# Optimization experiments

Measured on AMD Instinct MI355X. Metric: run time of the kernel, lower is better.

## Reference

```python
import jax, jax.numpy as jnp
import numpy as np

EMB_DIM = 128
MID = 192  # ceil(1.5 * emb_dim)
VOCAB = 3000
KCLS = 5
B = 16
S = 128
EPS = 1e-5


def _linear_init(k, fin, fout):
    k1, k2 = jax.random.split(k)
    bound = 1.0 / np.sqrt(fin)
    W = jax.random.uniform(k1, (fin, fout), minval=-bound, maxval=bound, dtype=jnp.float32)
    b = jax.random.uniform(k2, (fout,), minval=-bound, maxval=bound, dtype=jnp.float32)
    return W, b


def setup_inputs() -> dict:
    key = jax.random.key(0)
    ks = jax.random.split(key, 7)
    emb = jax.random.normal(ks[0], (VOCAB, EMB_DIM), dtype=jnp.float32)
    W1, b1 = _linear_init(ks[1], 2 * EMB_DIM, MID)   # encoder layer 1
    W2, b2 = _linear_init(ks[2], MID, EMB_DIM)       # encoder layer 2
    W3, b3 = _linear_init(ks[3], EMB_DIM, MID)       # decoder layer 1
    W4, b4 = _linear_init(ks[4], MID, 2 * EMB_DIM)   # decoder layer 2
    Wk, bk = _linear_init(ks[5], EMB_DIM, KCLS)      # soft head
    inputs = jax.random.randint(ks[6], (B, S), 0, VOCAB, dtype=jnp.int64)
    return dict(inputs=inputs, emb=emb, W1=W1, b1=b1, W2=W2, b2=b2,
                W3=W3, b3=b3, W4=W4, b4=b4, Wk=Wk, bk=bk)


def _forward(inputs, emb, W1, b1, W2, b2, W3, b3, W4, b4, Wk, bk):
    X = emb[inputs]                      # (B,S,m)
    Bs, Sl, m = X.shape
    bidx = jnp.arange(Bs)
    karr = jnp.arange(Sl)
    jarr = jnp.arange(Sl - 1)

    def step(carry, t):
        nodes, counts, acc = carry       # (B,S,m), (B,S), (B,)
        L = Sl - t                       # current active list length
        right, left = nodes[:, 1:], nodes[:, :-1]          # pair j = (node[j+1], node[j])
        y = (jnp.concatenate([right, left], -1) @ W1 + b1) @ W2 + b2   # (B,S-1,m)
        xx = (y @ W3 + b3) @ W4 + b4                                    # (B,S-1,2m)
        # torch cross_entropy with float-vector target: -sum(target * log_softmax(input))
        ls1 = -(right * jax.nn.log_softmax(xx[..., :m], -1)).sum(-1)
        ls2 = -(left * jax.nn.log_softmax(xx[..., m:], -1)).sum(-1)
        n1, n2 = counts[:, 1:], counts[:, :-1]
        loss = ((n1 + EPS) * ls1 + (n2 + EPS) * ls2) / (n1 + n2 + EPS)
        valid = jarr < (L - 1)                                          # only first L-1 pairs active
        idx = jnp.argmin(jnp.where(valid[None, :], loss, jnp.inf), axis=1)  # (B,)
        acc = acc + jnp.take_along_axis(loss, idx[:, None], 1)[:, 0]
        father_x = jnp.take_along_axis(y, idx[:, None, None], 1)[:, 0]  # (B,m)
        # faithful bug: lc = nodelist[idx-1] (python wrap to L-1 when idx==0), rc = nodelist[idx]
        lc_idx = jnp.where(idx == 0, L - 1, idx - 1)
        father_cnt = (jnp.take_along_axis(counts, idx[:, None], 1)[:, 0]
                      + jnp.take_along_axis(counts, lc_idx[:, None], 1)[:, 0])
        pos = jnp.maximum(idx - 1, 0)
        # new list: drop lc and rc, father lands at pos; gather map reproduces list insert/remove
        src = jnp.where((idx[:, None] == 0) | (karr[None, :] < idx[:, None] - 1),
                        karr[None, :], karr[None, :] + 1)
        src = jnp.minimum(src, Sl - 1)
        nodes = jnp.take_along_axis(nodes, src[:, :, None], 1).at[bidx, pos].set(father_x)
        counts = jnp.take_along_axis(counts, src, 1).at[bidx, pos].set(father_cnt)
        return (nodes, counts, acc), None

    init = (X, jnp.ones((Bs, Sl), X.dtype), jnp.zeros((Bs,), X.dtype))
    (nodes, counts, acc), _ = jax.lax.scan(step, init, jnp.arange(Sl - 1))
    pred = jnp.argmax(nodes[:, 0] @ Wk + bk, axis=-1)   # argmax softmax == argmax logits
    return pred, acc.sum() / Bs


def reference(inputs, emb, W1, b1, W2, b2, W3, b3, W4, b4, Wk, bk):
    return _forward(inputs, emb, W1, b1, W2, b2, W3, b3, W4, b4, Wk, bk)
```

## Files before the change

### kernel.cpp

```cpp
#include <hip/hip_runtime.h>
#include <math.h>

#define EMB 128
#define MID 192
#define SEQ 128
#define BATCH 16
#define NPAIR 127
#define KCLS 5
#define EPSF 1e-5f

#define OFF_WYT   0
#define OFF_BY    32768
#define OFF_WXX   32896
#define OFF_BXX   65664
#define OFF_NODES 65920
#define OFF_YC    328064
#define OFF_L0    588160

__global__ void k_comp(const float* __restrict__ W1, const float* __restrict__ b1,
                       const float* __restrict__ W2, const float* __restrict__ b2,
                       const float* __restrict__ W3, const float* __restrict__ b3,
                       const float* __restrict__ W4, const float* __restrict__ b4,
                       float* __restrict__ ws) {
    int tid = blockIdx.x * blockDim.x + threadIdx.x;
    if (tid < 32768) {
        int k = tid >> 7, o = tid & 127;
        float a = 0.f;
        for (int j = 0; j < MID; ++j) a += W1[k*MID+j] * W2[j*EMB+o];
        int q8 = k >> 5, jj = k & 31;
        ws[OFF_WYT + ((q8*128 + o) << 5) + jj] = a;
    } else if (tid < 65536) {
        int t = tid - 32768;
        int k = t >> 8, c = t & 255;
        float a = 0.f;
        for (int j = 0; j < MID; ++j) a += W3[k*MID+j] * W4[j*256+c];
        int h4 = k >> 5, jj = k & 31;
        ws[OFF_WXX + ((h4*256 + c) << 5) + jj] = a;
    } else if (tid < 65536 + 128) {
        int o = tid - 65536;
        float a = b2[o];
        for (int j = 0; j < MID; ++j) a += b1[j] * W2[j*EMB+o];
        ws[OFF_BY + o] = a;
    } else if (tid < 65536 + 128 + 256) {
        int o = tid - 65536 - 128;
        float a = b4[o];
        for (int j = 0; j < MID; ++j) a += b3[j] * W4[j*256+o];
        ws[OFF_BXX + o] = a;
    }
}

__global__ void k_nodes(const int* __restrict__ inp, const float* __restrict__ emb,
                        float* __restrict__ ws) {
    int tid = blockIdx.x * blockDim.x + threadIdx.x;
    if (tid >= BATCH*SEQ*EMB) return;
    int d = tid & 127;
    int bs = tid >> 7;
    int tok = inp[bs];
    ws[OFF_NODES + tid] = emb[tok*EMB + d];
}

__global__ void __launch_bounds__(1024) k_init(float* __restrict__ ws) {
    __shared__ float s_x[2][2*EMB];
    __shared__ float s_red[8][2][EMB];
    __shared__ float s_redx[4][2][256];
    __shared__ float s_y[2][EMB];
    __shared__ float s_by[EMB];
    __shared__ float s_bxx[2*EMB];
    __shared__ float s_ls[2][2];
    int tid = threadIdx.x;
    int b = blockIdx.x >> 4, g = blockIdx.x & 15;
    float4 wy8[8], wxx8[8];
    {
        const float4* gw = (const float4*)(ws + OFF_WYT) + (size_t)tid*8;
        #pragma unroll
        for (int i = 0; i < 8; ++i) wy8[i] = gw[i];
        const float4* gx = (const float4*)(ws + OFF_WXX) + (size_t)tid*8;
        #pragma unroll
        for (int i = 0; i < 8; ++i) wxx8[i] = gx[i];
    }
    if (tid < EMB) s_by[tid] = ws[OFF_BY + tid];
    if (tid < 2*EMB) s_bxx[tid] = ws[OFF_BXX + tid];
    const float* nodes = ws + OFF_NODES + (size_t)b*SEQ*EMB;
    float* yc = ws + OFF_YC + (size_t)b*NPAIR*EMB;
    int q8 = tid >> 7, o = tid & 127;
    int h4 = tid >> 8, c = tid & 255;
    __syncthreads();
    for (int it = 0; it < 4; ++it) {
        int base = g*8 + it*2;
        if (tid < 512) {
            int p_s = tid >> 8, kk = tid & 255;
            int j = base + p_s;
            int jj = j < NPAIR ? j : NPAIR - 1;
            s_x[p_s][kk] = nodes[(jj + (kk < 128 ? 1 : 0))*EMB + (kk & 127)];
        }
        __syncthreads();
        {
            const float4* sx4 = (const float4*)s_x;
            float a0 = 0.f, a1 = 0.f;
            #pragma unroll
            for (int i = 0; i < 8; ++i) {
                float4 w = wy8[i];
                float4 x0 = sx4[q8*8 + i];
                float4 x1 = sx4[64 + q8*8 + i];
                a0 += x0.x*w.x + x0.y*w.y + x0.z*w.z + x0.w*w.w;
                a1 += x1.x*w.x + x1.y*w.y + x1.z*w.z + x1.w*w.w;
            }
            s_red[q8][0][o] = a0;
            s_red[q8][1][o] = a1;
        }
        __syncthreads();
        if (tid < 256) {
            int p = tid >> 7, oo = tid & 127;
            float yv = s_by[oo];
            #pragma unroll
            for (int q = 0; q < 8; ++q) yv += s_red[q][p][oo];
            s_y[p][oo] = yv;
            int j2 = base + p;
            if (j2 < NPAIR) yc[(size_t)j2*EMB + oo] = yv;
        }
        __syncthreads();
        {
            const float4* sy4 = (const float4*)s_y;
            float c0 = 0.f, c1 = 0.f;
            #pragma unroll
            for (int i = 0; i < 8; ++i) {
                float4 w = wxx8[i];
                float4 y0 = sy4[h4*8 + i];
                float4 y1 = sy4[32 + h4*8 + i];
                c0 += y0.x*w.x + y0.y*w.y + y0.z*w.z + y0.w*w.w;
                c1 += y1.x*w.x + y1.y*w.y + y1.z*w.z + y1.w*w.w;
            }
            s_redx[h4][0][c] = c0;
            s_redx[h4][1][c] = c1;
        }
        __syncthreads();
        if (tid < 256) {
            int w = tid >> 6, lane = tid & 63;
            int p2 = w >> 1, h2 = w & 1;
            int cA = h2*128 + lane, cB = cA + 64;
            float v0 = s_redx[0][p2][cA] + s_redx[1][p2][cA] + s_redx[2][p2][cA] + s_redx[3][p2][cA] + s_bxx[cA];
            float v1 = s_redx[0][p2][cB] + s_redx[1][p2][cB] + s_redx[2][p2][cB] + s_redx[3][p2][cB] + s_bxx[cB];
            float m = fmaxf(v0, v1);
            for (int s = 32; s; s >>= 1) m = fmaxf(m, __shfl_xor(m, s, 64));
            float se = expf(v0 - m) + expf(v1 - m);
            for (int s = 32; s; s >>= 1) se += __shfl_xor(se, s, 64);
            float lse = m + logf(se);
            float o0 = s_x[p2][cA], o1 = s_x[p2][cB];
            float term = o0*(v0 - lse) + o1*(v1 - lse);
            for (int s = 32; s; s >>= 1) term += __shfl_xor(term, s, 64);
            if (lane == 0) s_ls[p2][h2] = -term;
        }
        __syncthreads();
        if (tid < 2) {
            int j2 = base + tid;
            if (j2 < NPAIR) {
                float l = ((1.f+EPSF)*s_ls[tid][0] + (1.f+EPSF)*s_ls[tid][1]) / (2.f + EPSF);
                ws[OFF_L0 + b*NPAIR + j2] = l;
            }
        }
        __syncthreads();
    }
}

__global__ void __launch_bounds__(1024) k_seq(float* __restrict__ ws,
                      const float* __restrict__ Wk, const float* __restrict__ bkv,
                      float* __restrict__ out) {
    __shared__ float s_nodes[SEQ*EMB];
    __shared__ float s_yc[NPAIR*EMB];
    __shared__ float s_red[8][2][EMB];
    __shared__ float s_redx[4][2][256];
    __shared__ float s_y[2][EMB];
    __shared__ float s_by[EMB];
    __shared__ float s_bxx[2*EMB];
    __shared__ float s_ls[2][2];
    __shared__ float s_loss[2][NPAIR];
    __shared__ float s_cnt[2][SEQ];
    __shared__ int   s_nslot[2][SEQ];
    __shared__ int   s_yslot[2][NPAIR];
    __shared__ int   s_q[2];
    __shared__ float s_wv[2];
    __shared__ int   s_wi[2];
    __shared__ float s_log[KCLS];

    int tid = threadIdx.x;
    int b = blockIdx.x;
    float4 wy8[8], wxx8[8];
    {
        const float4* gw = (const float4*)(ws + OFF_WYT) + (size_t)tid*8;
        #pragma unroll
        for (int i = 0; i < 8; ++i) wy8[i] = gw[i];
        const float4* gx = (const float4*)(ws + OFF_WXX) + (size_t)tid*8;
        #pragma unroll
        for (int i = 0; i < 8; ++i) wxx8[i] = gx[i];
    }
    {
        const float4* gn = (const float4*)(ws + OFF_NODES + (size_t)b*SEQ*EMB);
        float4* sn = (float4*)s_nodes;
        for (int i = tid; i < SEQ*EMB/4; i += 1024) sn[i] = gn[i];
        const float4* gy = (const float4*)(ws + OFF_YC + (size_t)b*NPAIR*EMB);
        float4* sy = (float4*)s_yc;
        for (int i = tid; i < NPAIR*EMB/4; i += 1024) sy[i] = gy[i];
    }
    if (tid < EMB) s_by[tid] = ws[OFF_BY + tid];
    if (tid < 2*EMB) s_bxx[tid] = ws[OFF_BXX + tid];
    if (tid < NPAIR) { s_loss[0][tid] = ws[OFF_L0 + b*NPAIR + tid]; s_yslot[0][tid] = tid; }
    if (tid < SEQ)   { s_cnt[0][tid] = 1.f; s_nslot[0][tid] = tid; }
    float acc = 0.f;
    int q8 = tid >> 7, o = tid & 127;
    int h4 = tid >> 8, c = tid & 255;
    __syncthreads();

    #pragma unroll 1
    for (int t = 0; t < NPAIR; ++t) {
        int L = SEQ - t;
        int cur = t & 1, nxt = cur ^ 1;
        if (t > 0) {
            {
                int r = (q8 < 4) ? 1 : 0;
                int slot0 = s_nslot[cur][s_q[0] + r];
                int slot1 = s_nslot[cur][s_q[1] + r];
                const float4* n4 = (const float4*)s_nodes;
                int sub = (q8 & 3) * 8;
                int base0 = slot0*32 + sub;
                int base1 = slot1*32 + sub;
                float a0 = 0.f, a1 = 0.f;
                #pragma unroll
                for (int i = 0; i < 8; ++i) {
                    float4 w = wy8[i];
                    float4 x0 = n4[base0 + i];
                    float4 x1 = n4[base1 + i];
                    a0 += x0.x*w.x + x0.y*w.y + x0.z*w.z + x0.w*w.w;
                    a1 += x1.x*w.x + x1.y*w.y + x1.z*w.z + x1.w*w.w;
                }
                s_red[q8][0][o] = a0;
                s_red[q8][1][o] = a1;
            }
            __syncthreads();
            if (tid < 256) {
                int p = tid >> 7, oo = tid & 127;
                float yv = s_by[oo];
                #pragma unroll
                for (int q = 0; q < 8; ++q) yv += s_red[q][p][oo];
                s_y[p][oo] = yv;
                s_yc[(size_t)s_yslot[cur][s_q[p]]*EMB + oo] = yv;
            }
            __syncthreads();
            {
                const float4* sy4 = (const float4*)s_y;
                float c0 = 0.f, c1 = 0.f;
                #pragma unroll
                for (int i = 0; i < 8; ++i) {
                    float4 w = wxx8[i];
                    float4 y0 = sy4[h4*8 + i];
                    float4 y1 = sy4[32 + h4*8 + i];
                    c0 += y0.x*w.x + y0.y*w.y + y0.z*w.z + y0.w*w.w;
                    c1 += y1.x*w.x + y1.y*w.y + y1.z*w.z + y1.w*w.w;
                }
                s_redx[h4][0][c] = c0;
                s_redx[h4][1][c] = c1;
            }
            __syncthreads();
            if (tid < 256) {
                int w = tid >> 6, lane = tid & 63;
                int p2 = w >> 1, h2 = w & 1;
                int cA = h2*128 + lane, cB = cA + 64;
                float v0 = s_redx[0][p2][cA] + s_redx[1][p2][cA] + s_redx[2][p2][cA] + s_redx[3][p2][cA] + s_bxx[cA];
                float v1 = s_redx[0][p2][cB] + s_redx[1][p2][cB] + s_redx[2][p2][cB] + s_redx[3][p2][cB] + s_bxx[cB];
                float m = fmaxf(v0, v1);
                for (int s = 32; s; s >>= 1) m = fmaxf(m, __shfl_xor(m, s, 64));
                float se = expf(v0 - m) + expf(v1 - m);
                for (int s = 32; s; s >>= 1) se += __shfl_xor(se, s, 64);
                float lse = m + logf(se);
                int slot = s_nslot[cur][s_q[p2] + (h2 == 0 ? 1 : 0)];
                float o0 = s_nodes[slot*EMB + lane];
                float o1 = s_nodes[slot*EMB + 64 + lane];
                float term = o0*(v0 - lse) + o1*(v1 - lse);
                for (int s = 32; s; s >>= 1) term += __shfl_xor(term, s, 64);
                if (lane == 0) s_ls[p2][h2] = -term;
            }
            __syncthreads();
        }
        if (tid < 128) {
            float v = INFINITY;
            if (tid < L-1) {
                v = s_loss[cur][tid];
                if (t > 0 && (tid == s_q[0] || tid == s_q[1])) {
                    int which = (tid == s_q[0]) ? 0 : 1;
                    float n1 = s_cnt[cur][tid+1], n2 = s_cnt[cur][tid];
                    v = ((n1+EPSF)*s_ls[which][0] + (n2+EPSF)*s_ls[which][1]) / (n1+n2+EPSF);
                    s_loss[cur][tid] = v;
                }
            }
            int ii = tid;
            for (int s = 32; s; s >>= 1) {
                float ov = __shfl_xor(v, s, 64);
                int   oi = __shfl_xor(ii, s, 64);
                if (ov < v || (ov == v && oi < ii)) { v = ov; ii = oi; }
            }
            if ((tid & 63) == 0) { s_wv[tid>>6] = v; s_wi[tid>>6] = ii; }
        }
        __syncthreads();
        {
            float bv0 = s_wv[0], bv1 = s_wv[1];
            int idx = (bv1 < bv0) ? s_wi[1] : s_wi[0];
            if (tid == 0) acc += fminf(bv0, bv1);
            int pos = idx > 0 ? idx - 1 : 0;
            bool doShift = (idx > 0);
            if (tid < 128) {
                int sC = (doShift && tid >= pos+1 && tid <= L-2) ? 1 : 0;
                float nc = s_cnt[cur][tid + sC];
                int   nn = s_nslot[cur][tid + sC];
                if (tid == pos) {
                    float fcnt = s_cnt[cur][idx] + s_cnt[cur][idx == 0 ? L-1 : idx-1];
                    nc = fcnt;
                }
                s_cnt[nxt][tid] = nc;
                s_nslot[nxt][tid] = nn;
                if (tid < NPAIR) {
                    int sL = (doShift && tid >= pos+1 && tid <= L-3) ? 1 : 0;
                    s_loss[nxt][tid]  = s_loss[cur][tid + sL];
                    s_yslot[nxt][tid] = s_yslot[cur][tid + sL];
                }
            } else if (tid < 256) {
                int d = tid - 128;
                int slotF = s_nslot[cur][pos];
                int ysI   = s_yslot[cur][idx];
                s_nodes[slotF*EMB + d] = s_yc[(size_t)ysI*EMB + d];
            } else if (tid == 256) {
                s_q[0] = (pos >= 1) ? pos - 1 : pos;
                s_q[1] = pos;
            }
        }
        __syncthreads();
    }
    if (tid < KCLS) {
        int slot0 = s_nslot[1][0];
        float a = bkv[tid];
        for (int k = 0; k < EMB; ++k) a += s_nodes[slot0*EMB + k] * Wk[k*KCLS + tid];
        s_log[tid] = a;
    }
    __syncthreads();
    if (tid == 0) {
        int best = 0;
        for (int cc = 1; cc < KCLS; ++cc) if (s_log[cc] > s_log[best]) best = cc;
        out[b] = (float)best;
        atomicAdd(&out[BATCH], acc * (1.f/16.f));
    }
}

extern "C" void kernel_launch(void* const* d_in, const int* in_sizes, int n_in,
                              void* d_out, int out_size, void* d_ws, size_t ws_size,
                              hipStream_t stream) {
    const int*   inp = (const int*)d_in[0];
    const float* emb = (const float*)d_in[1];
    const float* W1  = (const float*)d_in[2];
    const float* b1  = (const float*)d_in[3];
    const float* W2  = (const float*)d_in[4];
    const float* b2  = (const float*)d_in[5];
    const float* W3  = (const float*)d_in[6];
    const float* b3  = (const float*)d_in[7];
    const float* W4  = (const float*)d_in[8];
    const float* b4  = (const float*)d_in[9];
    const float* Wk  = (const float*)d_in[10];
    const float* bk  = (const float*)d_in[11];
    float* out = (float*)d_out;
    float* ws  = (float*)d_ws;

    hipMemsetAsync(d_out, 0, (size_t)out_size * sizeof(float), stream);

    k_comp<<<(65920 + 255) / 256, 256, 0, stream>>>(W1, b1, W2, b2, W3, b3, W4, b4, ws);
    k_nodes<<<(BATCH*SEQ*EMB + 255) / 256, 256, 0, stream>>>(inp, emb, ws);
    k_init<<<BATCH * 16, 1024, 0, stream>>>(ws);
    k_seq<<<BATCH, 1024, 0, stream>>>(ws, Wk, bk, out);
}
```

Baseline: 560.4 us.

## Decompose pair linear maps into per-node projections cached per slot

The composed encoder and decoder weights are split by input half, so each node gets cached left/right encoder projections and left/right decoder logit projections. A pair's y and logits then become sums of two per-node vectors plus a bias. In the sequential loop only the new father node is projected, using a single fused 128x768 matvec, instead of re-running two pair matvecs with cross-warp reductions. This removes one matvec stage and several barriers per step, but adds global-memory reads of cached projections in the critical loop, extra precompute kernels, and changes the floating-point summation order.

```diff
diff --git a/kernel.cpp b/kernel.cpp
--- a/kernel.cpp
+++ b/kernel.cpp
@@ -9,271 +9,243 @@
 #define KCLS 5
 #define EPSF 1e-5f
 
-#define OFF_WYT   0
-#define OFF_BY    32768
-#define OFF_WXX   32896
-#define OFF_BXX   65664
-#define OFF_NODES 65920
-#define OFF_YC    328064
-#define OFF_L0    588160
-
-__global__ void k_comp(const float* __restrict__ W1, const float* __restrict__ b1,
-                       const float* __restrict__ W2, const float* __restrict__ b2,
-                       const float* __restrict__ W3, const float* __restrict__ b3,
-                       const float* __restrict__ W4, const float* __restrict__ b4,
-                       float* __restrict__ ws) {
+#define OFF_WBIG  0
+#define OFF_BY    98304
+#define OFF_BXX2  98432
+#define OFF_WY    98688
+#define OFF_WXX   131456
+#define OFF_BXX   164224
+#define OFF_NODES 164480
+#define OFF_L0    426624
+#define OFF_L     428656
+#define OFF_R     690800
+#define OFF_UL    952944
+#define OFF_UR    1477232
+
+__global__ void k_comp1(const float* __restrict__ W1, const float* __restrict__ b1,
+                        const float* __restrict__ W2, const float* __restrict__ b2,
+                        const float* __restrict__ W3, const float* __restrict__ b3,
+                        const float* __restrict__ W4, const float* __restrict__ b4,
+                        const int* __restrict__ inp, const float* __restrict__ emb,
+                        float* __restrict__ ws) {
     int tid = blockIdx.x * blockDim.x + threadIdx.x;
     if (tid < 32768) {
         int k = tid >> 7, o = tid & 127;
         float a = 0.f;
         for (int j = 0; j < MID; ++j) a += W1[k*MID+j] * W2[j*EMB+o];
-        int q8 = k >> 5, jj = k & 31;
-        ws[OFF_WYT + ((q8*128 + o) << 5) + jj] = a;
+        ws[OFF_WY + k*128 + o] = a;
+        if (k >= 128) ws[OFF_WBIG + o*128 + (k-128)] = a;
+        else          ws[OFF_WBIG + (128+o)*128 + k] = a;
     } else if (tid < 65536) {
         int t = tid - 32768;
         int k = t >> 8, c = t & 255;
         float a = 0.f;
         for (int j = 0; j < MID; ++j) a += W3[k*MID+j] * W4[j*256+c];
-        int h4 = k >> 5, jj = k & 31;
-        ws[OFF_WXX + ((h4*256 + c) << 5) + jj] = a;
-    } else if (tid < 65536 + 128) {
+        ws[OFF_WXX + k*256 + c] = a;
+    } else if (tid < 65664) {
         int o = tid - 65536;
         float a = b2[o];
         for (int j = 0; j < MID; ++j) a += b1[j] * W2[j*EMB+o];
         ws[OFF_BY + o] = a;
-    } else if (tid < 65536 + 128 + 256) {
-        int o = tid - 65536 - 128;
+    } else if (tid < 65920) {
+        int o = tid - 65664;
         float a = b4[o];
         for (int j = 0; j < MID; ++j) a += b3[j] * W4[j*256+o];
         ws[OFF_BXX + o] = a;
-    }
-}
-
-__global__ void k_nodes(const int* __restrict__ inp, const float* __restrict__ emb,
-                        float* __restrict__ ws) {
+    } else if (tid < 65920 + BATCH*SEQ*EMB) {
+        int t2 = tid - 65920;
+        int d = t2 & 127, bs = t2 >> 7;
+        int tok = inp[bs];
+        ws[OFF_NODES + t2] = emb[tok*EMB + d];
+    }
+}
+
+__global__ void k_comp2(float* __restrict__ ws) {
     int tid = blockIdx.x * blockDim.x + threadIdx.x;
-    if (tid >= BATCH*SEQ*EMB) return;
-    int d = tid & 127;
-    int bs = tid >> 7;
-    int tok = inp[bs];
-    ws[OFF_NODES + tid] = emb[tok*EMB + d];
-}
-
-__global__ void __launch_bounds__(1024) k_init(float* __restrict__ ws) {
-    __shared__ float s_x[2][2*EMB];
-    __shared__ float s_red[8][2][EMB];
-    __shared__ float s_redx[4][2][256];
-    __shared__ float s_y[2][EMB];
-    __shared__ float s_by[EMB];
-    __shared__ float s_bxx[2*EMB];
-    __shared__ float s_ls[2][2];
+    if (tid < 32768) {
+        int k = tid >> 8, c = tid & 255;
+        float a = 0.f;
+        for (int m = 0; m < 128; ++m) a += ws[OFF_WY + (128+k)*128 + m] * ws[OFF_WXX + m*256 + c];
+        ws[OFF_WBIG + (256+c)*128 + k] = a;
+    } else if (tid < 65536) {
+        int t = tid - 32768;
+        int k = t >> 8, c = t & 255;
+        float a = 0.f;
+        for (int m = 0; m < 128; ++m) a += ws[OFF_WY + k*128 + m] * ws[OFF_WXX + m*256 + c];
+        ws[OFF_WBIG + (512+c)*128 + k] = a;
+    } else if (tid < 65792) {
+        int c = tid - 65536;
+        float a = ws[OFF_BXX + c];
+        for (int m = 0; m < 128; ++m) a += ws[OFF_BY + m] * ws[OFF_WXX + m*256 + c];
+        ws[OFF_BXX2 + c] = a;
+    }
+}
+
+__global__ void __launch_bounds__(768) k_cache(float* __restrict__ ws) {
+    __shared__ float s_x[EMB];
     int tid = threadIdx.x;
     int b = blockIdx.x >> 4, g = blockIdx.x & 15;
-    float4 wy8[8], wxx8[8];
+    float4 wb[32];
     {
-        const float4* gw = (const float4*)(ws + OFF_WYT) + (size_t)tid*8;
+        const float4* gw = (const float4*)(ws + OFF_WBIG) + (size_t)tid*32;
         #pragma unroll
-        for (int i = 0; i < 8; ++i) wy8[i] = gw[i];
-        const float4* gx = (const float4*)(ws + OFF_WXX) + (size_t)tid*8;
+        for (int i = 0; i < 32; ++i) wb[i] = gw[i];
+    }
+    const float* gnod = ws + OFF_NODES + (size_t)b*SEQ*EMB;
+    float* gL  = ws + OFF_L  + (size_t)b*SEQ*EMB;
+    float* gR  = ws + OFF_R  + (size_t)b*SEQ*EMB;
+    float* gUL = ws + OFF_UL + (size_t)b*SEQ*256;
+    float* gUR = ws + OFF_UR + (size_t)b*SEQ*256;
+    for (int i = 0; i < 8; ++i) {
+        int n = g*8 + i;
+        if (tid < EMB) s_x[tid] = gnod[n*EMB + tid];
+        __syncthreads();
+        float a0=0.f,a1=0.f,a2=0.f,a3=0.f;
+        const float4* f4 = (const float4*)s_x;
         #pragma unroll
-        for (int i = 0; i < 8; ++i) wxx8[i] = gx[i];
-    }
-    if (tid < EMB) s_by[tid] = ws[OFF_BY + tid];
-    if (tid < 2*EMB) s_bxx[tid] = ws[OFF_BXX + tid];
-    const float* nodes = ws + OFF_NODES + (size_t)b*SEQ*EMB;
-    float* yc = ws + OFF_YC + (size_t)b*NPAIR*EMB;
-    int q8 = tid >> 7, o = tid & 127;
-    int h4 = tid >> 8, c = tid & 255;
+        for (int ii = 0; ii < 8; ++ii) {
+            float4 w0 = wb[4*ii+0], x0 = f4[4*ii+0];
+            float4 w1 = wb[4*ii+1], x1 = f4[4*ii+1];
+            float4 w2 = wb[4*ii+2], x2 = f4[4*ii+2];
+            float4 w3 = wb[4*ii+3], x3 = f4[4*ii+3];
+            a0 += w0.x*x0.x + w0.y*x0.y + w0.z*x0.z + w0.w*x0.w;
+            a1 += w1.x*x1.x + w1.y*x1.y + w1.z*x1.z + w1.w*x1.w;
+            a2 += w2.x*x2.x + w2.y*x2.y + w2.z*x2.z + w2.w*x2.w;
+            a3 += w3.x*x3.x + w3.y*x3.y + w3.z*x3.z + w3.w*x3.w;
+        }
+        float o = (a0+a1)+(a2+a3);
+        if      (tid < 128) gL [n*EMB + tid]        = o;
+        else if (tid < 256) gR [n*EMB + tid-128]    = o;
+        else if (tid < 512) gUL[n*256 + tid-256]    = o;
+        else                gUR[n*256 + tid-512]    = o;
+        __syncthreads();
+    }
+}
+
+__global__ void __launch_bounds__(128) k_loss(float* __restrict__ ws) {
+    __shared__ float s_ls[2];
+    int tid = threadIdx.x;
+    int b = blockIdx.x / NPAIR, j = blockIdx.x % NPAIR;
+    int h2 = tid >> 6, lane = tid & 63;
+    const float* gUL = ws + OFF_UL + (size_t)b*SEQ*256;
+    const float* gUR = ws + OFF_UR + (size_t)b*SEQ*256;
+    const float* gnod = ws + OFF_NODES + (size_t)b*SEQ*EMB;
+    int cA = h2*128 + lane, cB = cA + 64;
+    float v0 = gUL[j*256+cA] + gUR[(j+1)*256+cA] + ws[OFF_BXX2+cA];
+    float v1 = gUL[j*256+cB] + gUR[(j+1)*256+cB] + ws[OFF_BXX2+cB];
+    float m = fmaxf(v0, v1);
+    for (int s = 32; s; s >>= 1) m = fmaxf(m, __shfl_xor(m, s, 64));
+    float se = expf(v0 - m) + expf(v1 - m);
+    for (int s = 32; s; s >>= 1) se += __shfl_xor(se, s, 64);
+    float lse = m + logf(se);
+    int slotD = j + (h2 == 0 ? 1 : 0);
+    float o0 = gnod[slotD*EMB + lane];
+    float o1 = gnod[slotD*EMB + 64 + lane];
+    float term = o0*(v0 - lse) + o1*(v1 - lse);
+    for (int s = 32; s; s >>= 1) term += __shfl_xor(term, s, 64);
+    if (lane == 0) s_ls[h2] = -term;
     __syncthreads();
-    for (int it = 0; it < 4; ++it) {
-        int base = g*8 + it*2;
-        if (tid < 512) {
-            int p_s = tid >> 8, kk = tid & 255;
-            int j = base + p_s;
-            int jj = j < NPAIR ? j : NPAIR - 1;
-            s_x[p_s][kk] = nodes[(jj + (kk < 128 ? 1 : 0))*EMB + (kk & 127)];
-        }
-        __syncthreads();
-        {
-            const float4* sx4 = (const float4*)s_x;
-            float a0 = 0.f, a1 = 0.f;
-            #pragma unroll
-            for (int i = 0; i < 8; ++i) {
-                float4 w = wy8[i];
-                float4 x0 = sx4[q8*8 + i];
-                float4 x1 = sx4[64 + q8*8 + i];
-                a0 += x0.x*w.x + x0.y*w.y + x0.z*w.z + x0.w*w.w;
-                a1 += x1.x*w.x + x1.y*w.y + x1.z*w.z + x1.w*w.w;
-            }
-            s_red[q8][0][o] = a0;
-            s_red[q8][1][o] = a1;
-        }
-        __syncthreads();
-        if (tid < 256) {
-            int p = tid >> 7, oo = tid & 127;
-            float yv = s_by[oo];
-            #pragma unroll
-            for (int q = 0; q < 8; ++q) yv += s_red[q][p][oo];
-            s_y[p][oo] = yv;
-            int j2 = base + p;
-            if (j2 < NPAIR) yc[(size_t)j2*EMB + oo] = yv;
-        }
-        __syncthreads();
-        {
-            const float4* sy4 = (const float4*)s_y;
-            float c0 = 0.f, c1 = 0.f;
-            #pragma unroll
-            for (int i = 0; i < 8; ++i) {
-                float4 w = wxx8[i];
-                float4 y0 = sy4[h4*8 + i];
-                float4 y1 = sy4[32 + h4*8 + i];
-                c0 += y0.x*w.x + y0.y*w.y + y0.z*w.z + y0.w*w.w;
-                c1 += y1.x*w.x + y1.y*w.y + y1.z*w.z + y1.w*w.w;
-            }
-            s_redx[h4][0][c] = c0;
-            s_redx[h4][1][c] = c1;
-        }
-        __syncthreads();
-        if (tid < 256) {
-            int w = tid >> 6, lane = tid & 63;
-            int p2 = w >> 1, h2 = w & 1;
-            int cA = h2*128 + lane, cB = cA + 64;
-            float v0 = s_redx[0][p2][cA] + s_redx[1][p2][cA] + s_redx[2][p2][cA] + s_redx[3][p2][cA] + s_bxx[cA];
-            float v1 = s_redx[0][p2][cB] + s_redx[1][p2][cB] + s_redx[2][p2][cB] + s_redx[3][p2][cB] + s_bxx[cB];
-            float m = fmaxf(v0, v1);
-            for (int s = 32; s; s >>= 1) m = fmaxf(m, __shfl_xor(m, s, 64));
-            float se = expf(v0 - m) + expf(v1 - m);
-            for (int s = 32; s; s >>= 1) se += __shfl_xor(se, s, 64);
-            float lse = m + logf(se);
-            float o0 = s_x[p2][cA], o1 = s_x[p2][cB];
-            float term = o0*(v0 - lse) + o1*(v1 - lse);
-            for (int s = 32; s; s >>= 1) term += __shfl_xor(term, s, 64);
-            if (lane == 0) s_ls[p2][h2] = -term;
-        }
-        __syncthreads();
-        if (tid < 2) {
-            int j2 = base + tid;
-            if (j2 < NPAIR) {
-                float l = ((1.f+EPSF)*s_ls[tid][0] + (1.f+EPSF)*s_ls[tid][1]) / (2.f + EPSF);
-                ws[OFF_L0 + b*NPAIR + j2] = l;
-            }
-        }
-        __syncthreads();
-    }
-}
-
-__global__ void __launch_bounds__(1024) k_seq(float* __restrict__ ws,
+    if (tid == 0) {
+        float l = ((1.f+EPSF)*s_ls[0] + (1.f+EPSF)*s_ls[1]) / (2.f + EPSF);
+        ws[OFF_L0 + b*NPAIR + j] = l;
+    }
+}
+
+__global__ void __launch_bounds__(768) k_seq(float* __restrict__ ws,
                       const float* __restrict__ Wk, const float* __restrict__ bkv,
                       float* __restrict__ out) {
     __shared__ float s_nodes[SEQ*EMB];
-    __shared__ float s_yc[NPAIR*EMB];
-    __shared__ float s_red[8][2][EMB];
-    __shared__ float s_redx[4][2][256];
-    __shared__ float s_y[2][EMB];
+    __shared__ float s_father[EMB];
+    __shared__ float s_Lf[EMB];
+    __shared__ float s_Rf[EMB];
+    __shared__ float s_ULf[256];
+    __shared__ float s_URf[256];
     __shared__ float s_by[EMB];
-    __shared__ float s_bxx[2*EMB];
+    __shared__ float s_bxx2[256];
     __shared__ float s_ls[2][2];
     __shared__ float s_loss[2][NPAIR];
     __shared__ float s_cnt[2][SEQ];
     __shared__ int   s_nslot[2][SEQ];
-    __shared__ int   s_yslot[2][NPAIR];
     __shared__ int   s_q[2];
+    __shared__ int   s_sFb[2];
     __shared__ float s_wv[2];
     __shared__ int   s_wi[2];
     __shared__ float s_log[KCLS];
 
     int tid = threadIdx.x;
     int b = blockIdx.x;
-    float4 wy8[8], wxx8[8];
+    float4 wb[32];
     {
-        const float4* gw = (const float4*)(ws + OFF_WYT) + (size_t)tid*8;
+        const float4* gw = (const float4*)(ws + OFF_WBIG) + (size_t)tid*32;
         #pragma unroll
-        for (int i = 0; i < 8; ++i) wy8[i] = gw[i];
-        const float4* gx = (const float4*)(ws + OFF_WXX) + (size_t)tid*8;
-        #pragma unroll
-        for (int i = 0; i < 8; ++i) wxx8[i] = gx[i];
-    }
+        for (int i = 0; i < 32; ++i) wb[i] = gw[i];
+    }
+    float* gnod = ws + OFF_NODES + (size_t)b*SEQ*EMB;
+    float* gL  = ws + OFF_L  + (size_t)b*SEQ*EMB;
+    float* gR  = ws + OFF_R  + (size_t)b*SEQ*EMB;
+    float* gUL = ws + OFF_UL + (size_t)b*SEQ*256;
+    float* gUR = ws + OFF_UR + (size_t)b*SEQ*256;
     {
-        const float4* gn = (const float4*)(ws + OFF_NODES + (size_t)b*SEQ*EMB);
+        const float4* gn4 = (const float4*)gnod;
         float4* sn = (float4*)s_nodes;
-        for (int i = tid; i < SEQ*EMB/4; i += 1024) sn[i] = gn[i];
-        const float4* gy = (const float4*)(ws + OFF_YC + (size_t)b*NPAIR*EMB);
-        float4* sy = (float4*)s_yc;
-        for (int i = tid; i < NPAIR*EMB/4; i += 1024) sy[i] = gy[i];
+        for (int i = tid; i < SEQ*EMB/4; i += 768) sn[i] = gn4[i];
     }
     if (tid < EMB) s_by[tid] = ws[OFF_BY + tid];
-    if (tid < 2*EMB) s_bxx[tid] = ws[OFF_BXX + tid];
-    if (tid < NPAIR) { s_loss[0][tid] = ws[OFF_L0 + b*NPAIR + tid]; s_yslot[0][tid] = tid; }
-    if (tid < SEQ)   { s_cnt[0][tid] = 1.f; s_nslot[0][tid] = tid; }
+    if (tid < 256) s_bxx2[tid] = ws[OFF_BXX2 + tid];
+    if (tid < NPAIR) s_loss[0][tid] = ws[OFF_L0 + b*NPAIR + tid];
+    if (tid < SEQ) { s_cnt[0][tid] = 1.f; s_nslot[0][tid] = tid; }
+    if (tid == 0) { s_sFb[0] = -1; s_sFb[1] = -1; }
     float acc = 0.f;
-    int q8 = tid >> 7, o = tid & 127;
-    int h4 = tid >> 8, c = tid & 255;
     __syncthreads();
 
     #pragma unroll 1
     for (int t = 0; t < NPAIR; ++t) {
         int L = SEQ - t;
-        int cur = t & 1, nxt = cur ^ 1;
+        int cur = t & 1;
+        int prevPar = (t + 1) & 1;
+        int sF = s_sFb[prevPar];
         if (t > 0) {
             {
-                int r = (q8 < 4) ? 1 : 0;
-                int slot0 = s_nslot[cur][s_q[0] + r];
-                int slot1 = s_nslot[cur][s_q[1] + r];
-                const float4* n4 = (const float4*)s_nodes;
-                int sub = (q8 & 3) * 8;
-                int base0 = slot0*32 + sub;
-                int base1 = slot1*32 + sub;
-                float a0 = 0.f, a1 = 0.f;
+                float a0=0.f,a1=0.f,a2=0.f,a3=0.f;
+                const float4* f4 = (const float4*)s_father;
                 #pragma unroll
-                for (int i = 0; i < 8; ++i) {
-                    float4 w = wy8[i];
-                    float4 x0 = n4[base0 + i];
-                    float4 x1 = n4[base1 + i];
-                    a0 += x0.x*w.x + x0.y*w.y + x0.z*w.z + x0.w*w.w;
-                    a1 += x1.x*w.x + x1.y*w.y + x1.z*w.z + x1.w*w.w;
+                for (int ii = 0; ii < 8; ++ii) {
+                    float4 w0 = wb[4*ii+0], x0 = f4[4*ii+0];
+                    float4 w1 = wb[4*ii+1], x1 = f4[4*ii+1];
+                    float4 w2 = wb[4*ii+2], x2 = f4[4*ii+2];
+                    float4 w3 = wb[4*ii+3], x3 = f4[4*ii+3];
+                    a0 += w0.x*x0.x + w0.y*x0.y + w0.z*x0.z + w0.w*x0.w;
+                    a1 += w1.x*x1.x + w1.y*x1.y + w1.z*x1.z + w1.w*x1.w;
+                    a2 += w2.x*x2.x + w2.y*x2.y + w2.z*x2.z + w2.w*x2.w;
+                    a3 += w3.x*x3.x + w3.y*x3.y + w3.z*x3.z + w3.w*x3.w;
                 }
-                s_red[q8][0][o] = a0;
-                s_red[q8][1][o] = a1;
-            }
-            __syncthreads();
-            if (tid < 256) {
-                int p = tid >> 7, oo = tid & 127;
-                float yv = s_by[oo];
-                #pragma unroll
-                for (int q = 0; q < 8; ++q) yv += s_red[q][p][oo];
-                s_y[p][oo] = yv;
-                s_yc[(size_t)s_yslot[cur][s_q[p]]*EMB + oo] = yv;
-            }
-            __syncthreads();
-            {
-                const float4* sy4 = (const float4*)s_y;
-                float c0 = 0.f, c1 = 0.f;
-                #pragma unroll
-                for (int i = 0; i < 8; ++i) {
-                    float4 w = wxx8[i];
-                    float4 y0 = sy4[h4*8 + i];
-                    float4 y1 = sy4[32 + h4*8 + i];
-                    c0 += y0.x*w.x + y0.y*w.y + y0.z*w.z + y0.w*w.w;
-                    c1 += y1.x*w.x + y1.y*w.y + y1.z*w.z + y1.w*w.w;
-                }
-                s_redx[h4][0][c] = c0;
-                s_redx[h4][1][c] = c1;
+                float o = (a0+a1)+(a2+a3);
+                if      (tid < 128) { gL [sF*EMB + tid]      = o; s_Lf [tid]     = o; }
+                else if (tid < 256) { gR [sF*EMB + tid-128]  = o; s_Rf [tid-128] = o; }
+                else if (tid < 512) { gUL[sF*256 + tid-256]  = o; s_ULf[tid-256] = o; }
+                else                { gUR[sF*256 + tid-512]  = o; s_URf[tid-512] = o; }
             }
             __syncthreads();
             if (tid < 256) {
                 int w = tid >> 6, lane = tid & 63;
                 int p2 = w >> 1, h2 = w & 1;
+                int q = s_q[p2];
+                int slotL = s_nslot[cur][q], slotR = s_nslot[cur][q+1];
                 int cA = h2*128 + lane, cB = cA + 64;
-                float v0 = s_redx[0][p2][cA] + s_redx[1][p2][cA] + s_redx[2][p2][cA] + s_redx[3][p2][cA] + s_bxx[cA];
-                float v1 = s_redx[0][p2][cB] + s_redx[1][p2][cB] + s_redx[2][p2][cB] + s_redx[3][p2][cB] + s_bxx[cB];
+                float ulA = (slotL == sF) ? s_ULf[cA] : gUL[slotL*256 + cA];
+                float ulB = (slotL == sF) ? s_ULf[cB] : gUL[slotL*256 + cB];
+                float urA = (slotR == sF) ? s_URf[cA] : gUR[slotR*256 + cA];
+                float urB = (slotR == sF) ? s_URf[cB] : gUR[slotR*256 + cB];
+                float v0 = ulA + urA + s_bxx2[cA];
+                float v1 = ulB + urB + s_bxx2[cB];
                 float m = fmaxf(v0, v1);
                 for (int s = 32; s; s >>= 1) m = fmaxf(m, __shfl_xor(m, s, 64));
                 float se = expf(v0 - m) + expf(v1 - m);
                 for (int s = 32; s; s >>= 1) se += __shfl_xor(se, s, 64);
                 float lse = m + logf(se);
-                int slot = s_nslot[cur][s_q[p2] + (h2 == 0 ? 1 : 0)];
-                float o0 = s_nodes[slot*EMB + lane];
-                float o1 = s_nodes[slot*EMB + 64 + lane];
+                int slotD = (h2 == 0) ? slotR : slotL;
+                float o0 = s_nodes[slotD*EMB + lane];
+                float o1 = s_nodes[slotD*EMB + 64 + lane];
                 float term = o0*(v0 - lse) + o1*(v1 - lse);
                 for (int s = 32; s; s >>= 1) term += __shfl_xor(term, s, 64);
                 if (lane == 0) s_ls[p2][h2] = -term;
@@ -305,30 +277,33 @@
             int idx = (bv1 < bv0) ? s_wi[1] : s_wi[0];
             if (tid == 0) acc += fminf(bv0, bv1);
             int pos = idx > 0 ? idx - 1 : 0;
+            int nxt = cur ^ 1;
             bool doShift = (idx > 0);
             if (tid < 128) {
                 int sC = (doShift && tid >= pos+1 && tid <= L-2) ? 1 : 0;
                 float nc = s_cnt[cur][tid + sC];
                 int   nn = s_nslot[cur][tid + sC];
-                if (tid == pos) {
-                    float fcnt = s_cnt[cur][idx] + s_cnt[cur][idx == 0 ? L-1 : idx-1];
-                    nc = fcnt;
-                }
+                if (tid == pos) nc = s_cnt[cur][idx] + s_cnt[cur][idx == 0 ? L-1 : idx-1];
                 s_cnt[nxt][tid] = nc;
                 s_nslot[nxt][tid] = nn;
                 if (tid < NPAIR) {
                     int sL = (doShift && tid >= pos+1 && tid <= L-3) ? 1 : 0;
-                    s_loss[nxt][tid]  = s_loss[cur][tid + sL];
-                    s_yslot[nxt][tid] = s_yslot[cur][tid + sL];
+                    s_loss[nxt][tid] = s_loss[cur][tid + sL];
                 }
             } else if (tid < 256) {
                 int d = tid - 128;
-                int slotF = s_nslot[cur][pos];
-                int ysI   = s_yslot[cur][idx];
-                s_nodes[slotF*EMB + d] = s_yc[(size_t)ysI*EMB + d];
+                int slotI  = s_nslot[cur][idx];
+                int slotI1 = s_nslot[cur][idx+1];
+                int slotF  = s_nslot[cur][pos];
+                float fL = (slotI  == sF) ? s_Lf[d] : gL[slotI*EMB + d];
+                float fR = (slotI1 == sF) ? s_Rf[d] : gR[slotI1*EMB + d];
+                float fa = fL + fR + s_by[d];
+                s_father[d] = fa;
+                s_nodes[slotF*EMB + d] = fa;
             } else if (tid == 256) {
                 s_q[0] = (pos >= 1) ? pos - 1 : pos;
                 s_q[1] = pos;
+                s_sFb[t & 1] = s_nslot[cur][pos];
             }
         }
         __syncthreads();
@@ -368,8 +343,10 @@
 
     hipMemsetAsync(d_out, 0, (size_t)out_size * sizeof(float), stream);
 
-    k_comp<<<(65920 + 255) / 256, 256, 0, stream>>>(W1, b1, W2, b2, W3, b3, W4, b4, ws);
-    k_nodes<<<(BATCH*SEQ*EMB + 255) / 256, 256, 0, stream>>>(inp, emb, ws);
-    k_init<<<BATCH * 16, 1024, 0, stream>>>(ws);
-    k_seq<<<BATCH, 1024, 0, stream>>>(ws, Wk, bk, out);
-}
+    int n1 = 65920 + BATCH*SEQ*EMB;
+    k_comp1<<<(n1 + 255) / 256, 256, 0, stream>>>(W1, b1, W2, b2, W3, b3, W4, b4, inp, emb, ws);
+    k_comp2<<<(65792 + 255) / 256, 256, 0, stream>>>(ws);
+    k_cache<<<BATCH * 16, 768, 0, stream>>>(ws);
+    k_loss<<<BATCH * NPAIR, 128, 0, stream>>>(ws);
+    k_seq<<<BATCH, 768, 0, stream>>>(ws, Wk, bk, out);
+}
```

Result: slower. 650.8 us (+16.1%).
